# Kernel tuning notes

Measured on AMD Instinct MI355X. Metric: run time of the kernel, lower is better.

The kernel has to match this reference:

```python
import jax, jax.numpy as jnp
import numpy as np

NUM_USERS = 100000
NUM_ITEMS = 50000
N_NODES = NUM_USERS + NUM_ITEMS
LATENT_DIM = 64
N_LAYERS = 3
N_EDGES = 1200000
K = 0.8  # laplace-k blending: Graph = (1-k)*I + k*G


def setup_inputs() -> dict:
    key = jax.random.key(0)
    k1, k2, k3, k4, k5, k6, k7 = jax.random.split(key, 7)
    # xavier_uniform for embeddings: bound = sqrt(6/(fan_in+fan_out))
    bu = float(np.sqrt(6.0 / (NUM_USERS + LATENT_DIM)))
    bi = float(np.sqrt(6.0 / (NUM_ITEMS + LATENT_DIM)))
    user_emb = jax.random.uniform(k1, (NUM_USERS, LATENT_DIM), jnp.float32, -bu, bu)
    item_emb = jax.random.uniform(k2, (NUM_ITEMS, LATENT_DIM), jnp.float32, -bi, bi)
    edge_row = jax.random.randint(k3, (N_EDGES,), 0, N_NODES)
    edge_col = jax.random.randint(k4, (N_EDGES,), 0, N_NODES)
    # normalized-adjacency-like positive values
    edge_val = jax.random.uniform(k5, (N_EDGES,), jnp.float32) * 0.01
    users = jax.random.randint(k6, (4096,), 0, NUM_USERS)
    items = jax.random.randint(k7, (4096,), 0, NUM_ITEMS)
    return {"users": users, "items": items, "edge_row": edge_row,
            "edge_col": edge_col, "edge_val": edge_val,
            "user_emb": user_emb, "item_emb": item_emb}


def _spmm(edge_row, edge_col, edge_val, x):
    # y = G @ x via gather + segment_sum over static edge list
    msgs = edge_val[:, None] * x[edge_col]  # [E, D]
    return jax.ops.segment_sum(msgs, edge_row, num_segments=N_NODES)


def _computer(user_emb, item_emb, edge_row, edge_col, edge_val):
    all_emb = jnp.concatenate([user_emb, item_emb], axis=0)  # [N, D]
    acc = all_emb  # running sum of layer embeddings (mean taken at end)
    emb = all_emb
    for _ in range(N_LAYERS):
        # Graph = (1-K)*I + K*G, so spmm(Graph, emb) = (1-K)*emb + K*G@emb
        emb = (1.0 - K) * emb + K * _spmm(edge_row, edge_col, edge_val, emb)
        acc = acc + emb
    light_out = acc / (N_LAYERS + 1)  # mean over stacked layer embeddings
    return light_out[:NUM_USERS], light_out[NUM_USERS:]


def reference(users, items, edge_row, edge_col, edge_val, user_emb, item_emb):
    all_users, all_items = _computer(user_emb, item_emb, edge_row, edge_col, edge_val)
    u = all_users[users]  # [B, D]
    i = all_items[items]  # [B, D]
    gamma = jnp.sum(u * i, axis=1)  # [B]
    return gamma
```

## Files before the change

kernel.cpp:

```cpp
#include <hip/hip_runtime.h>
#include <hip/hip_fp16.h>
#include <stdint.h>
#include <string.h>


#define NUM_USERS 100000
#define NUM_ITEMS 50000
#define N_NODES   150000
#define DIM       64
#define N_EDGES   1200000
#define ND        (N_NODES * DIM)
#define NB        4096
#define NSAMP     (2 * NB)

#define ELL_W     24
#define NBKT      640
#define RPB       235
#define NROWS_PAD (NBKT * RPB)
#define BCAP      2176
#define SCAP      11
#define OVF_CAP   512

#define K1_THREADS     1024
#define K1_EDGE_BLOCKS 256
#define K1_ROUNDS      2
#define K1_MARK_BLOCKS 8
#define K1_CVT_BLOCKS  128
#define K2_EXP_BLOCKS  2048
#define K2_CPY_BLOCKS  586
#define SPMM_BLOCKS    9375
#define ACC_BLOCKS     512

__device__ __forceinline__ int h2i(__half2 h) { int r; memcpy(&r, &h, 4); return r; }
__device__ __forceinline__ __half2 i2h(int i) { __half2 h; memcpy(&h, &i, 4); return h; }

__device__ __forceinline__ float4 loadh4(const __half* p) {
    int2 v = *(const int2*)p;
    float2 a = __half22float2(i2h(v.x));
    float2 b = __half22float2(i2h(v.y));
    return make_float4(a.x, a.y, b.x, b.y);
}
__device__ __forceinline__ void storeh4(__half* p, float4 v) {
    int2 o;
    o.x = h2i(__floats2half2_rn(v.x, v.y));
    o.y = h2i(__floats2half2_rn(v.z, v.w));
    *(int2*)p = o;
}
__device__ __forceinline__ float4 f4fma(float v, float4 x, float4 a) {
    a.x += v * x.x; a.y += v * x.y; a.z += v * x.z; a.w += v * x.w;
    return a;
}

__global__ __launch_bounds__(K1_THREADS)
void k1_kernel(const int* __restrict__ erow,
               const int* __restrict__ ecol,
               const float* __restrict__ evalv,
               const int* __restrict__ users,
               const int* __restrict__ items,
               const float* __restrict__ ue,
               const float* __restrict__ ie,
               int* __restrict__ gtails,
               int2* __restrict__ barr,
               int4* __restrict__ ovf,
               int* __restrict__ ovf_cnt,
               unsigned char* __restrict__ mask3,
               __half* __restrict__ xh) {
    __shared__ int2 stage[NBKT * SCAP];
    __shared__ int  scnt[NBKT];
    if (blockIdx.x < K1_EDGE_BLOCKS) {
        for (int k = threadIdx.x; k < NBKT; k += K1_THREADS) scnt[k] = 0;
        __syncthreads();
        for (int rnd = 0; rnd < K1_ROUNDS; ++rnd) {
            int base = ((rnd * K1_EDGE_BLOCKS + (int)blockIdx.x) * K1_THREADS
                        + (int)threadIdx.x) * 4;
            if (base < N_EDGES) {
                int4   r4 = *(const int4*)(erow + base);
                int4   c4 = *(const int4*)(ecol + base);
                float4 v4 = *(const float4*)(evalv + base);
                int   rr[4] = {r4.x, r4.y, r4.z, r4.w};
                int   cc[4] = {c4.x, c4.y, c4.z, c4.w};
                float vv[4] = {v4.x, v4.y, v4.z, v4.w};
                #pragma unroll
                for (int u = 0; u < 4; ++u) {
                    int b    = rr[u] / RPB;
                    int rloc = rr[u] - b * RPB;
                    int2 rec = make_int2(cc[u] | (rloc << 18), __float_as_int(vv[u]));
                    int s = atomicAdd(&scnt[b], 1);
                    if (s < SCAP) {
                        stage[b * SCAP + s] = rec;
                    } else {
                        atomicSub(&scnt[b], 1);
                        int gp = atomicAdd(&gtails[b], 1);
                        if (gp < BCAP) barr[(size_t)b * BCAP + gp] = rec;
                        else { int q = atomicAdd(ovf_cnt, 1);
                               if (q < OVF_CAP)
                                   ovf[q] = make_int4(rr[u], cc[u], __float_as_int(vv[u]), 0); }
                    }
                }
            }
            __syncthreads();
            for (int b = threadIdx.x; b < NBKT; b += K1_THREADS) {
                int c = scnt[b];
                if (c >= 8) {
                    int gp = atomicAdd(&gtails[b], 8);
                    if (gp + 8 <= BCAP) {
                        int2* dst = barr + (size_t)b * BCAP + gp;
                        #pragma unroll
                        for (int i = 0; i < 8; ++i) dst[i] = stage[b * SCAP + i];
                    } else {
                        for (int i = 0; i < 8; ++i) {
                            int2 rc = stage[b * SCAP + i];
                            if (gp + i < BCAP) barr[(size_t)b * BCAP + gp + i] = rc;
                            else { int q = atomicAdd(ovf_cnt, 1);
                                   if (q < OVF_CAP)
                                       ovf[q] = make_int4(b * RPB + (rc.x >> 18),
                                                          rc.x & 0x3FFFF, rc.y, 0); }
                        }
                    }
                    c -= 8;
                    for (int i = 0; i < c; ++i)
                        stage[b * SCAP + i] = stage[b * SCAP + 8 + i];
                    scnt[b] = c;
                }
            }
            __syncthreads();
        }
        for (int b = threadIdx.x; b < NBKT; b += K1_THREADS) {
            int c = scnt[b];
            if (c > 0) {
                int gp = atomicAdd(&gtails[b], c);
                for (int i = 0; i < c; ++i) {
                    int2 rc = stage[b * SCAP + i];
                    if (gp + i < BCAP) barr[(size_t)b * BCAP + gp + i] = rc;
                    else { int q = atomicAdd(ovf_cnt, 1);
                           if (q < OVF_CAP)
                               ovf[q] = make_int4(b * RPB + (rc.x >> 18),
                                                  rc.x & 0x3FFFF, rc.y, 0); }
                }
            }
        }
    } else if (blockIdx.x < K1_EDGE_BLOCKS + K1_MARK_BLOCKS) {
        int i = ((int)blockIdx.x - K1_EDGE_BLOCKS) * K1_THREADS + (int)threadIdx.x;
        if (i < NB)         mask3[users[i]] = 1;
        else if (i < NSAMP) mask3[NUM_USERS + items[i - NB]] = 1;
    } else {
        const int n4  = ND / 4;
        const int nu4 = NUM_USERS * DIM / 4;
        int i = ((int)blockIdx.x - K1_EDGE_BLOCKS - K1_MARK_BLOCKS) * K1_THREADS
                + (int)threadIdx.x;
        const int stride = K1_CVT_BLOCKS * K1_THREADS;
        int2* xh4 = (int2*)xh;
        for (; i < n4; i += stride) {
            float4 v = (i < nu4) ? ((const float4*)ue)[i]
                                 : ((const float4*)ie)[i - nu4];
            int2 o;
            o.x = h2i(__floats2half2_rn(v.x, v.y));
            o.y = h2i(__floats2half2_rn(v.z, v.w));
            xh4[i] = o;
        }
    }
}

__global__ __launch_bounds__(256)
void k2_kernel(const int* __restrict__ erow,
               const int* __restrict__ ecol,
               const int* __restrict__ gtails,
               const int2* __restrict__ barr,
               int* __restrict__ counts,
               int2* __restrict__ ell,
               int4* __restrict__ ovf,
               int* __restrict__ ovf_cnt,
               const unsigned char* __restrict__ mask3,
               unsigned char* __restrict__ mask2) {
    __shared__ __align__(16) int2 lell[RPB * ELL_W];
    __shared__ int lcnt[RPB];
    if (blockIdx.x < NBKT) {
        const int bkt   = blockIdx.x;
        const int rbase = bkt * RPB;
        for (int k = threadIdx.x; k < RPB; k += 256) lcnt[k] = 0;
        __syncthreads();
        int n = gtails[bkt];
        n = n < BCAP ? n : BCAP;
        for (int e = threadIdx.x; e < n; e += 256) {
            int2 rec = barr[(size_t)bkt * BCAP + e];
            int col  = rec.x & 0x3FFFF;
            int rloc = rec.x >> 18;
            int slot = atomicAdd(&lcnt[rloc], 1);
            if (slot < ELL_W)
                lell[rloc * ELL_W + slot] = make_int2(col, rec.y);
            else { int q = atomicAdd(ovf_cnt, 1);
                   if (q < OVF_CAP) ovf[q] = make_int4(rbase + rloc, col, rec.y, 0); }
        }
        __syncthreads();
        int4* g4 = (int4*)(ell + (size_t)rbase * ELL_W);
        const int4* l4 = (const int4*)lell;
        for (int k = threadIdx.x; k < RPB * ELL_W / 2; k += 256) g4[k] = l4[k];
        for (int k = threadIdx.x; k < RPB; k += 256) counts[rbase + k] = lcnt[k];
    } else if (blockIdx.x < NBKT + K2_EXP_BLOCKS) {
        int i = ((int)blockIdx.x - NBKT) * 256 + (int)threadIdx.x;
        const int stride = K2_EXP_BLOCKS * 256;
        for (; i < N_EDGES; i += stride)
            if (mask3[erow[i]]) mask2[ecol[i]] = 1;
    } else {
        int i = ((int)blockIdx.x - NBKT - K2_EXP_BLOCKS) * 256 + (int)threadIdx.x;
        if (i < N_NODES && mask3[i]) mask2[i] = 1;
    }
}

template<bool MASKED, bool ACC_STORE>
__global__ void spmm_kernel(const int* __restrict__ counts,
                            const int2* __restrict__ ell,
                            const __half* __restrict__ xsrc,
                            const float* __restrict__ ue,
                            const float* __restrict__ ie,
                            const unsigned char* __restrict__ mask,
                            const int* __restrict__ ovf_cnt,
                            const int4* __restrict__ ovf,
                            const int* __restrict__ users,
                            const int* __restrict__ items,
                            float* __restrict__ acc_small,
                            __half* __restrict__ xout) {
    const int wid  = threadIdx.x >> 6;
    const int lane = threadIdx.x & 63;
    const int g    = lane >> 4;
    const int t    = lane & 15;

    if (blockIdx.x < SPMM_BLOCKS) {
        const int row = blockIdx.x * 16 + wid * 4 + g;
        bool active = true;
        if (MASKED) active = mask[row] != 0;
        int cnt = 0;
        if (active) {
            cnt = counts[row];
            cnt = cnt < ELL_W ? cnt : ELL_W;
        }
        const int2* ep = ell + (size_t)row * ELL_W;
        float4 a0 = {0,0,0,0}, a1 = {0,0,0,0}, a2 = {0,0,0,0}, a3 = {0,0,0,0};
        int j = 0;
        for (; j + 4 <= cnt; j += 4) {
            int4 cv0 = *(const int4*)(ep + j);
            int4 cv1 = *(const int4*)(ep + j + 2);
            float4 x0 = loadh4(xsrc + (size_t)cv0.x * DIM + t * 4);
            float4 x1 = loadh4(xsrc + (size_t)cv0.z * DIM + t * 4);
            float4 x2 = loadh4(xsrc + (size_t)cv1.x * DIM + t * 4);
            float4 x3 = loadh4(xsrc + (size_t)cv1.z * DIM + t * 4);
            a0 = f4fma(__int_as_float(cv0.y), x0, a0);
            a1 = f4fma(__int_as_float(cv0.w), x1, a1);
            a2 = f4fma(__int_as_float(cv1.y), x2, a2);
            a3 = f4fma(__int_as_float(cv1.w), x3, a3);
        }
        for (; j + 2 <= cnt; j += 2) {
            int4 cv = *(const int4*)(ep + j);
            float4 x0 = loadh4(xsrc + (size_t)cv.x * DIM + t * 4);
            float4 x1 = loadh4(xsrc + (size_t)cv.z * DIM + t * 4);
            a0 = f4fma(__int_as_float(cv.y), x0, a0);
            a1 = f4fma(__int_as_float(cv.w), x1, a1);
        }
        if (j < cnt) {
            int2 cv = ep[j];
            float4 xv = loadh4(xsrc + (size_t)cv.x * DIM + t * 4);
            a0 = f4fma(__int_as_float(cv.y), xv, a0);
        }
        int novf = *ovf_cnt;
        if (novf > 0) {
            novf = novf < OVF_CAP ? novf : OVF_CAP;
            for (int k = 0; k < novf; ++k) {
                int4 o = ovf[k];
                if (active && o.x == row) {
                    float4 xv = loadh4(xsrc + (size_t)o.y * DIM + t * 4);
                    a0 = f4fma(__int_as_float(o.z), xv, a0);
                }
            }
        }
        if (active) {
            float4 self = loadh4(xsrc + (size_t)row * DIM + t * 4);
            float4 r;
            r.x = 0.2f * self.x + 0.8f * ((a0.x + a1.x) + (a2.x + a3.x));
            r.y = 0.2f * self.y + 0.8f * ((a0.y + a1.y) + (a2.y + a3.y));
            r.z = 0.2f * self.z + 0.8f * ((a0.z + a1.z) + (a2.z + a3.z));
            r.w = 0.2f * self.w + 0.8f * ((a0.w + a1.w) + (a2.w + a3.w));
            storeh4(xout + (size_t)row * DIM + t * 4, r);
        }
    } else {
        const int s = (blockIdx.x - SPMM_BLOCKS) * 16 + wid * 4 + g;
        const int node = (s < NB) ? users[s] : (NUM_USERS + items[s - NB]);
        float4* ap = (float4*)(acc_small + (size_t)s * DIM + t * 4);
        if (ACC_STORE) {
            const float* p = (node < NUM_USERS) ? ue + (size_t)node * DIM
                                                : ie + (size_t)(node - NUM_USERS) * DIM;
            *ap = *(const float4*)(p + t * 4);
        } else {
            float4 v = loadh4(xsrc + (size_t)node * DIM + t * 4);
            float4 a = *ap;
            a.x += v.x; a.y += v.y; a.z += v.z; a.w += v.w;
            *ap = a;
        }
    }
}

__global__ void dot_kernel(const int* __restrict__ users,
                           const int* __restrict__ items,
                           const float* __restrict__ acc_small,
                           const __half* __restrict__ emb3,
                           float* __restrict__ out) {
    int w = (blockIdx.x * blockDim.x + threadIdx.x) >> 6;
    int lane = threadIdx.x & 63;
    if (w >= NB) return;
    int u  = users[w];
    int it = items[w];
    float au = acc_small[w * DIM + lane]
             + __half2float(emb3[(size_t)u * DIM + lane]);
    float ai = acc_small[(NB + w) * DIM + lane]
             + __half2float(emb3[(size_t)(NUM_USERS + it) * DIM + lane]);
    float p = au * ai;
    #pragma unroll
    for (int o = 32; o > 0; o >>= 1) p += __shfl_down(p, o, 64);
    if (lane == 0) out[w] = p * (1.0f / 16.0f);
}

extern "C" void kernel_launch(void* const* d_in, const int* in_sizes, int n_in,
                              void* d_out, int out_size, void* d_ws, size_t ws_size,
                              hipStream_t stream) {
    const int*   users = (const int*)  d_in[0];
    const int*   items = (const int*)  d_in[1];
    const int*   erow  = (const int*)  d_in[2];
    const int*   ecol  = (const int*)  d_in[3];
    const float* evalv = (const float*)d_in[4];
    const float* ue    = (const float*)d_in[5];
    const float* ie    = (const float*)d_in[6];
    float* out = (float*)d_out;

    __half* xh        = (__half*)d_ws;
    __half* emb_a     = xh + ND;
    __half* emb_b     = emb_a + ND;
    int2*   barr      = (int2*)emb_a;
    float*  acc_small = (float*)(emb_b + ND);
    int2*   ell       = (int2*)(acc_small + NSAMP * DIM);
    int*    counts    = (int*)(ell + (size_t)NROWS_PAD * ELL_W);
    int*    gtails    = counts + NROWS_PAD;
    int*    ovf_cnt   = gtails + NBKT;
    int4*   ovf       = (int4*)(((uintptr_t)(ovf_cnt + 1) + 15) & ~(uintptr_t)15);
    unsigned char* mask3 = (unsigned char*)(ovf + OVF_CAP);
    unsigned char* mask2 = mask3 + N_NODES;

    size_t zbytes = (size_t)((mask2 + N_NODES) - (unsigned char*)gtails);
    hipMemsetAsync(gtails, 0, zbytes, stream);

    k1_kernel<<<K1_EDGE_BLOCKS + K1_MARK_BLOCKS + K1_CVT_BLOCKS, K1_THREADS, 0, stream>>>(
        erow, ecol, evalv, users, items, ue, ie,
        gtails, barr, ovf, ovf_cnt, mask3, xh);

    k2_kernel<<<NBKT + K2_EXP_BLOCKS + K2_CPY_BLOCKS, 256, 0, stream>>>(
        erow, ecol, gtails, barr, counts, ell, ovf, ovf_cnt, mask3, mask2);

    spmm_kernel<false, true><<<SPMM_BLOCKS + ACC_BLOCKS, 256, 0, stream>>>(
        counts, ell, xh, ue, ie, nullptr, ovf_cnt, ovf,
        users, items, acc_small, emb_a);

    spmm_kernel<true, false><<<SPMM_BLOCKS + ACC_BLOCKS, 256, 0, stream>>>(
        counts, ell, emb_a, nullptr, nullptr, mask2, ovf_cnt, ovf,
        users, items, acc_small, emb_b);

    spmm_kernel<true, false><<<SPMM_BLOCKS + ACC_BLOCKS, 256, 0, stream>>>(
        counts, ell, emb_b, nullptr, nullptr, mask3, ovf_cnt, ovf,
        users, items, acc_small, emb_a);

    dot_kernel<<<(NB * 64 + 255) / 256, 256, 0, stream>>>(
        users, items, acc_small, emb_a, out);
}
```

Before: 209.1 us.

## Fuse ELL construction with the first SpMM layer using the shared-memory ELL

Each bucket block now runs the first propagation layer for its rows right after building its ELL slice in shared memory. It reads neighbor indices from LDS instead of global memory, and one full SpMM launch disappears. The accumulator initialisation from the fp32 embeddings moves into the same kernel. The bucket staging buffer no longer aliases emb_a, which is now written in that kernel. In exchange, the first layer runs on only 640 LDS-heavy blocks looping over 15 row groups, so latency hiding for the gathers may drop.

```diff
diff --git a/kernel.cpp b/kernel.cpp
--- a/kernel.cpp
+++ b/kernel.cpp
@@ -26,8 +26,11 @@
 #define K1_ROUNDS      2
 #define K1_MARK_BLOCKS 8
 #define K1_CVT_BLOCKS  128
-#define K2_EXP_BLOCKS  2048
-#define K2_CPY_BLOCKS  586
+
+#define S1_ACC_BLOCKS  512
+#define S1_EXP_BLOCKS  2048
+#define S1_CPY_BLOCKS  586
+
 #define SPMM_BLOCKS    9375
 #define ACC_BLOCKS     512
 
@@ -162,18 +165,30 @@
 }
 
 __global__ __launch_bounds__(256)
-void k2_kernel(const int* __restrict__ erow,
+void s1_kernel(const int* __restrict__ erow,
                const int* __restrict__ ecol,
                const int* __restrict__ gtails,
                const int2* __restrict__ barr,
+               const __half* __restrict__ xh,
+               const float* __restrict__ ue,
+               const float* __restrict__ ie,
                int* __restrict__ counts,
                int2* __restrict__ ell,
                int4* __restrict__ ovf,
                int* __restrict__ ovf_cnt,
                const unsigned char* __restrict__ mask3,
-               unsigned char* __restrict__ mask2) {
+               unsigned char* __restrict__ mask2,
+               const int* __restrict__ users,
+               const int* __restrict__ items,
+               float* __restrict__ acc_small,
+               __half* __restrict__ emb_out) {
     __shared__ __align__(16) int2 lell[RPB * ELL_W];
     __shared__ int lcnt[RPB];
+    const int wid  = threadIdx.x >> 6;
+    const int lane = threadIdx.x & 63;
+    const int g    = lane >> 4;
+    const int t    = lane & 15;
+
     if (blockIdx.x < NBKT) {
         const int bkt   = blockIdx.x;
         const int rbase = bkt * RPB;
@@ -192,27 +207,85 @@
                    if (q < OVF_CAP) ovf[q] = make_int4(rbase + rloc, col, rec.y, 0); }
         }
         __syncthreads();
-        int4* g4 = (int4*)(ell + (size_t)rbase * ELL_W);
-        const int4* l4 = (const int4*)lell;
-        for (int k = threadIdx.x; k < RPB * ELL_W / 2; k += 256) g4[k] = l4[k];
-        for (int k = threadIdx.x; k < RPB; k += 256) counts[rbase + k] = lcnt[k];
-    } else if (blockIdx.x < NBKT + K2_EXP_BLOCKS) {
-        int i = ((int)blockIdx.x - NBKT) * 256 + (int)threadIdx.x;
-        const int stride = K2_EXP_BLOCKS * 256;
+        {
+            int4* g4 = (int4*)(ell + (size_t)rbase * ELL_W);
+            const int4* l4 = (const int4*)lell;
+            for (int k = threadIdx.x; k < RPB * ELL_W / 2; k += 256) g4[k] = l4[k];
+            for (int k = threadIdx.x; k < RPB; k += 256) counts[rbase + k] = lcnt[k];
+        }
+        int novf = *ovf_cnt;
+        novf = novf < OVF_CAP ? novf : OVF_CAP;
+        for (int k = 0; k < 15; ++k) {
+            int rloc = wid * 4 + g + 16 * k;
+            if (rloc >= RPB) break;
+            int row = rbase + rloc;
+            if (row >= N_NODES) continue;
+            int cnt = lcnt[rloc];
+            cnt = cnt < ELL_W ? cnt : ELL_W;
+            const int2* ep = &lell[rloc * ELL_W];
+            float4 a0 = {0,0,0,0}, a1 = {0,0,0,0}, a2 = {0,0,0,0}, a3 = {0,0,0,0};
+            int j = 0;
+            for (; j + 4 <= cnt; j += 4) {
+                int4 cv0 = *(const int4*)(ep + j);
+                int4 cv1 = *(const int4*)(ep + j + 2);
+                float4 x0 = loadh4(xh + (size_t)cv0.x * DIM + t * 4);
+                float4 x1 = loadh4(xh + (size_t)cv0.z * DIM + t * 4);
+                float4 x2 = loadh4(xh + (size_t)cv1.x * DIM + t * 4);
+                float4 x3 = loadh4(xh + (size_t)cv1.z * DIM + t * 4);
+                a0 = f4fma(__int_as_float(cv0.y), x0, a0);
+                a1 = f4fma(__int_as_float(cv0.w), x1, a1);
+                a2 = f4fma(__int_as_float(cv1.y), x2, a2);
+                a3 = f4fma(__int_as_float(cv1.w), x3, a3);
+            }
+            for (; j + 2 <= cnt; j += 2) {
+                int4 cv = *(const int4*)(ep + j);
+                float4 x0 = loadh4(xh + (size_t)cv.x * DIM + t * 4);
+                float4 x1 = loadh4(xh + (size_t)cv.z * DIM + t * 4);
+                a0 = f4fma(__int_as_float(cv.y), x0, a0);
+                a1 = f4fma(__int_as_float(cv.w), x1, a1);
+            }
+            if (j < cnt) {
+                int2 cv = ep[j];
+                float4 xv = loadh4(xh + (size_t)cv.x * DIM + t * 4);
+                a0 = f4fma(__int_as_float(cv.y), xv, a0);
+            }
+            for (int q = 0; q < novf; ++q) {
+                int4 o = ovf[q];
+                if (o.x == row) {
+                    float4 xv = loadh4(xh + (size_t)o.y * DIM + t * 4);
+                    a0 = f4fma(__int_as_float(o.z), xv, a0);
+                }
+            }
+            float4 self = loadh4(xh + (size_t)row * DIM + t * 4);
+            float4 r;
+            r.x = 0.2f * self.x + 0.8f * ((a0.x + a1.x) + (a2.x + a3.x));
+            r.y = 0.2f * self.y + 0.8f * ((a0.y + a1.y) + (a2.y + a3.y));
+            r.z = 0.2f * self.z + 0.8f * ((a0.z + a1.z) + (a2.z + a3.z));
+            r.w = 0.2f * self.w + 0.8f * ((a0.w + a1.w) + (a2.w + a3.w));
+            storeh4(emb_out + (size_t)row * DIM + t * 4, r);
+        }
+    } else if (blockIdx.x < NBKT + S1_ACC_BLOCKS) {
+        const int s = ((int)blockIdx.x - NBKT) * 16 + wid * 4 + g;
+        const int node = (s < NB) ? users[s] : (NUM_USERS + items[s - NB]);
+        const float* p = (node < NUM_USERS) ? ue + (size_t)node * DIM
+                                            : ie + (size_t)(node - NUM_USERS) * DIM;
+        *(float4*)(acc_small + (size_t)s * DIM + t * 4) = *(const float4*)(p + t * 4);
+    } else if (blockIdx.x < NBKT + S1_ACC_BLOCKS + S1_EXP_BLOCKS) {
+        int i = ((int)blockIdx.x - NBKT - S1_ACC_BLOCKS) * 256 + (int)threadIdx.x;
+        const int stride = S1_EXP_BLOCKS * 256;
         for (; i < N_EDGES; i += stride)
             if (mask3[erow[i]]) mask2[ecol[i]] = 1;
     } else {
-        int i = ((int)blockIdx.x - NBKT - K2_EXP_BLOCKS) * 256 + (int)threadIdx.x;
+        int i = ((int)blockIdx.x - NBKT - S1_ACC_BLOCKS - S1_EXP_BLOCKS) * 256
+                + (int)threadIdx.x;
         if (i < N_NODES && mask3[i]) mask2[i] = 1;
     }
 }
 
-template<bool MASKED, bool ACC_STORE>
+template<bool ACC_STORE>
 __global__ void spmm_kernel(const int* __restrict__ counts,
                             const int2* __restrict__ ell,
                             const __half* __restrict__ xsrc,
-                            const float* __restrict__ ue,
-                            const float* __restrict__ ie,
                             const unsigned char* __restrict__ mask,
                             const int* __restrict__ ovf_cnt,
                             const int4* __restrict__ ovf,
@@ -227,8 +300,7 @@
 
     if (blockIdx.x < SPMM_BLOCKS) {
         const int row = blockIdx.x * 16 + wid * 4 + g;
-        bool active = true;
-        if (MASKED) active = mask[row] != 0;
+        bool active = mask[row] != 0;
         int cnt = 0;
         if (active) {
             cnt = counts[row];
@@ -284,17 +356,12 @@
     } else {
         const int s = (blockIdx.x - SPMM_BLOCKS) * 16 + wid * 4 + g;
         const int node = (s < NB) ? users[s] : (NUM_USERS + items[s - NB]);
+        float4 v = loadh4(xsrc + (size_t)node * DIM + t * 4);
         float4* ap = (float4*)(acc_small + (size_t)s * DIM + t * 4);
-        if (ACC_STORE) {
-            const float* p = (node < NUM_USERS) ? ue + (size_t)node * DIM
-                                                : ie + (size_t)(node - NUM_USERS) * DIM;
-            *ap = *(const float4*)(p + t * 4);
-        } else {
-            float4 v = loadh4(xsrc + (size_t)node * DIM + t * 4);
-            float4 a = *ap;
-            a.x += v.x; a.y += v.y; a.z += v.z; a.w += v.w;
-            *ap = a;
-        }
+        float4 a = *ap;
+        a.x += v.x; a.y += v.y; a.z += v.z; a.w += v.w;
+        *ap = a;
+        (void)ACC_STORE;
     }
 }
 
@@ -333,9 +400,9 @@
     __half* xh        = (__half*)d_ws;
     __half* emb_a     = xh + ND;
     __half* emb_b     = emb_a + ND;
-    int2*   barr      = (int2*)emb_a;
     float*  acc_small = (float*)(emb_b + ND);
-    int2*   ell       = (int2*)(acc_small + NSAMP * DIM);
+    int2*   barr      = (int2*)(acc_small + NSAMP * DIM);
+    int2*   ell       = barr + (size_t)NBKT * BCAP;
     int*    counts    = (int*)(ell + (size_t)NROWS_PAD * ELL_W);
     int*    gtails    = counts + NROWS_PAD;
     int*    ovf_cnt   = gtails + NBKT;
@@ -350,19 +417,16 @@
         erow, ecol, evalv, users, items, ue, ie,
         gtails, barr, ovf, ovf_cnt, mask3, xh);
 
-    k2_kernel<<<NBKT + K2_EXP_BLOCKS + K2_CPY_BLOCKS, 256, 0, stream>>>(
-        erow, ecol, gtails, barr, counts, ell, ovf, ovf_cnt, mask3, mask2);
-
-    spmm_kernel<false, true><<<SPMM_BLOCKS + ACC_BLOCKS, 256, 0, stream>>>(
-        counts, ell, xh, ue, ie, nullptr, ovf_cnt, ovf,
-        users, items, acc_small, emb_a);
-
-    spmm_kernel<true, false><<<SPMM_BLOCKS + ACC_BLOCKS, 256, 0, stream>>>(
-        counts, ell, emb_a, nullptr, nullptr, mask2, ovf_cnt, ovf,
+    s1_kernel<<<NBKT + S1_ACC_BLOCKS + S1_EXP_BLOCKS + S1_CPY_BLOCKS, 256, 0, stream>>>(
+        erow, ecol, gtails, barr, xh, ue, ie, counts, ell, ovf, ovf_cnt,
+        mask3, mask2, users, items, acc_small, emb_a);
+
+    spmm_kernel<false><<<SPMM_BLOCKS + ACC_BLOCKS, 256, 0, stream>>>(
+        counts, ell, emb_a, mask2, ovf_cnt, ovf,
         users, items, acc_small, emb_b);
 
-    spmm_kernel<true, false><<<SPMM_BLOCKS + ACC_BLOCKS, 256, 0, stream>>>(
-        counts, ell, emb_b, nullptr, nullptr, mask3, ovf_cnt, ovf,
+    spmm_kernel<false><<<SPMM_BLOCKS + ACC_BLOCKS, 256, 0, stream>>>(
+        counts, ell, emb_b, mask3, ovf_cnt, ovf,
         users, items, acc_small, emb_a);
 
     dot_kernel<<<(NB * 64 + 255) / 256, 256, 0, stream>>>(
```

New measurement: 212.0 us. About the same (+1.4%).
